# Kernel optimization log

Measured on AMD Instinct MI355X. Metric: run time of the kernel, lower is better.

The kernel has to match this reference:

```python
import jax, jax.numpy as jnp
import numpy as np
import math

N, E, D, H, L, DIN, NEP = 20000, 320000, 128, 8, 4, 16, 4
DFF = 4 * D
DH = D // H
SCALE = 1.0 / math.sqrt(DH)


def _ln(x, s, b, eps=1e-5):
    mu = x.mean(-1, keepdims=True)
    var = ((x - mu) ** 2).mean(-1, keepdims=True)
    return (x - mu) * jax.lax.rsqrt(var + eps) * s + b


def _attn(h, src, dst, ew, Wq, Wk, Wv, Wo, Wo_b):
    n = h.shape[0]
    Q = (h @ Wq).reshape(n, H, DH)
    K = (h @ Wk).reshape(n, H, DH)
    V = (h @ Wv).reshape(n, H, DH)
    # per-edge scores: [E, H]; ew is sigmoid(edge_feat.sum(-1, keepdims)) -> [E, 1]
    scores = (Q[src] * K[dst]).sum(-1) * SCALE * ew
    msg = V[dst] * scores[:, :, None]                       # [E, H, DH]
    sums = jax.ops.segment_sum(msg, dst, num_segments=n)    # [N, H, DH]
    cnt = jax.ops.segment_sum(jnp.ones((msg.shape[0],), h.dtype), dst, num_segments=n)
    out = sums / jnp.maximum(cnt, 1.0)[:, None, None]       # segment-mean (zeros if no edges)
    return out.reshape(n, D) @ Wo + Wo_b


def setup_inputs() -> dict:
    key = jax.random.key(0)
    ks = iter(jax.random.split(key, 40))
    rn = lambda *s: jax.random.normal(next(ks), s, jnp.float32) * 0.02
    inp = {
        'x': jax.random.normal(next(ks), (N, DIN), jnp.float32),
        'edge_index': jax.random.randint(next(ks), (2, E), 0, N),
        'edge_attr': jax.random.normal(next(ks), (E, 1), jnp.float32),
        'in_w': rn(DIN, D), 'in_b': jnp.zeros((D,)),
        'ee_w1': rn(1, D // 4), 'ee_b1': jnp.zeros((D // 4,)),
        'ee_w2': rn(D // 4, D // 2), 'ee_b2': jnp.zeros((D // 2,)),
        'Wq': rn(L, D, D), 'Wk': rn(L, D, D), 'Wv': rn(L, D, D),
        'Wo': rn(L, D, D), 'Wo_b': jnp.zeros((L, D)),
        'ff_w1': rn(L, D, DFF), 'ff_b1': jnp.zeros((L, DFF)),
        'ff_w2': rn(L, DFF, D), 'ff_b2': jnp.zeros((L, D)),
        'ln1_s': jnp.ones((L, D)), 'ln1_b': jnp.zeros((L, D)),
        'ln2_s': jnp.ones((L, D)), 'ln2_b': jnp.zeros((L, D)),
        'ec_w1': rn(D * 2 + D // 2, D), 'ec_b1': jnp.zeros((D,)),
        'ec_w2': rn(D, D // 2), 'ec_b2': jnp.zeros((D // 2,)),
        'ec_w3': rn(D // 2, 1), 'ec_b3': jnp.zeros((1,)),
        'pp_w1': rn(D * 2 + D // 2, D), 'pp_b1': jnp.zeros((D,)),
        'pp_w2': rn(D, D // 2), 'pp_b2': jnp.zeros((D // 2,)),
        'pp_w3': rn(D // 2, NEP), 'pp_b3': jnp.zeros((NEP,)),
    }
    return inp


def reference(x, edge_index, edge_attr, in_w, in_b, ee_w1, ee_b1, ee_w2, ee_b2,
              Wq, Wk, Wv, Wo, Wo_b, ff_w1, ff_b1, ff_w2, ff_b2,
              ln1_s, ln1_b, ln2_s, ln2_b,
              ec_w1, ec_b1, ec_w2, ec_b2, ec_w3, ec_b3,
              pp_w1, pp_b1, pp_w2, pp_b2, pp_w3, pp_b3):
    src, dst = edge_index[0], edge_index[1]
    h = x @ in_w + in_b                                     # [N, D]
    edge_feat = jax.nn.relu(edge_attr @ ee_w1 + ee_b1) @ ee_w2 + ee_b2  # [E, D/2]
    ew = jax.nn.sigmoid(edge_feat.sum(-1, keepdims=True))   # [E, 1]
    for l in range(L):
        a = _attn(h, src, dst, ew, Wq[l], Wk[l], Wv[l], Wo[l], Wo_b[l])
        h = _ln(h + a, ln1_s[l], ln1_b[l])
        f = jax.nn.relu(h @ ff_w1[l] + ff_b1[l]) @ ff_w2[l] + ff_b2[l]
        h = _ln(h + f, ln2_s[l], ln2_b[l])
    ef = jnp.concatenate([h[src], h[dst], edge_feat], axis=1)  # [E, 2.5*D]
    z = jax.nn.relu(ef @ ec_w1 + ec_b1)
    z = jax.nn.relu(z @ ec_w2 + ec_b2)
    edge_logits = (z @ ec_w3 + ec_b3).squeeze(-1)
    p = jax.nn.relu(ef @ pp_w1 + pp_b1)
    p = jax.nn.relu(p @ pp_w2 + pp_b2)
    edge_params = jax.nn.softplus(p @ pp_w3 + pp_b3) + 1e-6
    return edge_logits, edge_params
```

## Files before the change

### kernel.cpp

```cpp
#include <hip/hip_runtime.h>
#include <hip/hip_bf16.h>
#include <math.h>

#define N_NODES 20000
#define N_EDGES 320000
#define D 128
#define DFF 512
#define DIN 16
#define NLAYER 4
#define SCALE 0.25f
#define KE1 288

typedef __hip_bfloat16 bf16;
typedef __attribute__((ext_vector_type(8))) __bf16 bf16x8_t;
typedef __attribute__((ext_vector_type(4))) float f32x4;

__global__ void k_input_proj(const float* __restrict__ x, const float* __restrict__ in_w,
                             const float* __restrict__ in_b, float* __restrict__ h,
                             __bf16* __restrict__ h_bf) {
  int node = blockIdx.x;
  int j = threadIdx.x;
  __shared__ float xs[DIN];
  if (j < DIN) xs[j] = x[node * DIN + j];
  __syncthreads();
  float acc = in_b[j];
  for (int k = 0; k < DIN; ++k) acc = fmaf(xs[k], in_w[k * D + j], acc);
  h[(size_t)node * D + j] = acc;
  h_bf[(size_t)node * D + j] = (__bf16)acc;
}

__global__ void k_edge_prep(const float* __restrict__ ea, const float* __restrict__ w1,
                            const float* __restrict__ b1, const float* __restrict__ w2,
                            const float* __restrict__ b2, const int* __restrict__ dst,
                            float* __restrict__ ew, float* __restrict__ cnt) {
  __shared__ float rs[32], w1s[32], b1s[32];
  __shared__ float b2sum;
  int tid = threadIdx.x;
  if (tid < 32) {
    float s = 0.f;
    for (int j = 0; j < 64; ++j) s += w2[tid * 64 + j];
    rs[tid] = s;
    w1s[tid] = w1[tid];
    b1s[tid] = b1[tid];
  }
  if (tid == 0) {
    float s = 0.f;
    for (int j = 0; j < 64; ++j) s += b2[j];
    b2sum = s;
  }
  __syncthreads();
  int e = blockIdx.x * blockDim.x + tid;
  if (e >= N_EDGES) return;
  float a = ea[e];
  float s = b2sum;
  for (int i = 0; i < 32; ++i) {
    float t = fmaxf(fmaf(a, w1s[i], b1s[i]), 0.f);
    s = fmaf(t, rs[i], s);
  }
  ew[e] = 1.f / (1.f + expf(-s));
  atomicAdd(&cnt[dst[e]], 1.f);
}

__global__ void k_cvt_all(const float* __restrict__ Wq, const float* __restrict__ Wk,
                          const float* __restrict__ Wv, const float* __restrict__ ffw1,
                          const float* __restrict__ ffw2, const float* __restrict__ Wo,
                          const float* __restrict__ ecw2, const float* __restrict__ ppw2,
                          __bf16* __restrict__ wqkvT, __bf16* __restrict__ w1T,
                          __bf16* __restrict__ w2T, __bf16* __restrict__ woT,
                          __bf16* __restrict__ w2ET, __bf16* __restrict__ w2PT) {
  int t = blockIdx.x * 256 + threadIdx.x;
  if (t < 196608) {
    int l = t / 49152, u = t % 49152;
    int m = u / 16384, v = u % 16384;
    int n = v / 128, k = v % 128;
    const float* W = (m == 0) ? Wq : (m == 1) ? Wk : Wv;
    wqkvT[t] = (__bf16)W[l * 16384 + k * 128 + n];
  } else if (t < 196608 + 262144) {
    int u = t - 196608;
    int l = u / 65536, v = u % 65536;
    int n = v / 128, k = v % 128;
    w1T[u] = (__bf16)ffw1[l * 65536 + k * 512 + n];
  } else if (t < 458752 + 262144) {
    int u = t - 458752;
    int l = u / 65536, v = u % 65536;
    int n = v / 512, k = v % 512;
    w2T[u] = (__bf16)ffw2[l * 65536 + k * 128 + n];
  } else if (t < 720896 + 65536) {
    int u = t - 720896;
    int l = u / 16384, v = u % 16384;
    int n = v / 128, k = v % 128;
    woT[u] = (__bf16)Wo[l * 16384 + k * 128 + n];
  } else if (t < 786432 + 8192) {
    int u = t - 786432;
    int n = u / 128, k = u % 128;
    w2ET[u] = (__bf16)ecw2[k * 64 + n];
  } else if (t < 794624 + 8192) {
    int u = t - 794624;
    int n = u / 128, k = u % 128;
    w2PT[u] = (__bf16)ppw2[k * 64 + n];
  }
}

__global__ void k_prep(const float* __restrict__ ec_w1, const float* __restrict__ ec_b1,
                       const float* __restrict__ pp_w1, const float* __restrict__ pp_b1,
                       const float* __restrict__ ee_w2, const float* __restrict__ ee_b2,
                       __bf16* __restrict__ w1ET, __bf16* __restrict__ w1PT,
                       float* __restrict__ b1Ep, float* __restrict__ b1Pp) {
  int tid = threadIdx.x;
  int p = tid >> 7, n = tid & 127;
  const float* w1 = p ? pp_w1 : ec_w1;
  const float* bb = p ? pp_b1 : ec_b1;
  __bf16* wT = p ? w1PT : w1ET;
  float* bo = p ? b1Pp : b1Ep;
  for (int k = 0; k < 256; ++k) wT[n * KE1 + k] = (__bf16)w1[k * 128 + n];
  for (int i = 0; i < 32; ++i) {
    float m = 0.f;
    for (int j = 0; j < 64; ++j) m = fmaf(ee_w2[i * 64 + j], w1[(256 + j) * 128 + n], m);
    wT[n * KE1 + 256 + i] = (__bf16)m;
  }
  float b = bb[n];
  for (int j = 0; j < 64; ++j) b = fmaf(ee_b2[j], w1[(256 + j) * 128 + n], b);
  bo[n] = b;
}

__global__ __launch_bounds__(256) void k_qkv(const __bf16* __restrict__ h_bf,
                                             const __bf16* __restrict__ wT,
                                             __bf16* __restrict__ Q, __bf16* __restrict__ K,
                                             __bf16* __restrict__ V) {
  int tid = threadIdx.x, wv = tid >> 6, lane = tid & 63;
  int lr = lane & 15, lk = (lane >> 4) * 8, g4 = (lane >> 4) * 4;
  int n0 = blockIdx.x * 16;
  const __bf16* hp = h_bf + (size_t)(n0 + lr) * D;
  f32x4 acc[6];
#pragma unroll
  for (int j = 0; j < 6; ++j) acc[j] = (f32x4){0.f, 0.f, 0.f, 0.f};
#pragma unroll
  for (int ks = 0; ks < 4; ++ks) {
    bf16x8_t aF = *(const bf16x8_t*)&hp[ks * 32 + lk];
#pragma unroll
    for (int j = 0; j < 6; ++j) {
      int nb = wv * 6 + j;
      bf16x8_t bF = *(const bf16x8_t*)&wT[(nb * 16 + lr) * 128 + ks * 32 + lk];
      acc[j] = __builtin_amdgcn_mfma_f32_16x16x32_bf16(aF, bF, acc[j], 0, 0, 0);
    }
  }
#pragma unroll
  for (int j = 0; j < 6; ++j) {
    int nb = wv * 6 + j;
    int m = nb >> 3;
    __bf16* out = (m == 0) ? Q : (m == 1) ? K : V;
#pragma unroll
    for (int r = 0; r < 4; ++r)
      out[(size_t)(n0 + g4 + r) * D + (nb & 7) * 16 + lr] = (__bf16)acc[j][r];
  }
}

__global__ void k_edge_attn(const int* __restrict__ src, const int* __restrict__ dst,
                            const float* __restrict__ ew, const __bf16* __restrict__ Q,
                            const __bf16* __restrict__ K, float* __restrict__ sc) {
  int t = blockIdx.x * blockDim.x + threadIdx.x;
  if (t >= N_EDGES * 8) return;
  int e = t >> 3, hd = t & 7;
  int s = src[e], d = dst[e];
  const __bf16* q = Q + (size_t)s * D + hd * 16;
  const __bf16* k = K + (size_t)d * D + hd * 16;
  bf16x8_t q0 = *(const bf16x8_t*)q, q1 = *(const bf16x8_t*)(q + 8);
  bf16x8_t k0 = *(const bf16x8_t*)k, k1 = *(const bf16x8_t*)(k + 8);
  float p = 0.f;
#pragma unroll
  for (int i = 0; i < 8; ++i) p = fmaf((float)q0[i], (float)k0[i], p);
#pragma unroll
  for (int i = 0; i < 8; ++i) p = fmaf((float)q1[i], (float)k1[i], p);
  atomicAdd(&sc[d * 8 + hd], p * SCALE * ew[e]);
}

__global__ __launch_bounds__(256) void k_node(
    float* __restrict__ sc, const float* __restrict__ cnt, const __bf16* __restrict__ Vin,
    float* __restrict__ h, __bf16* __restrict__ h_bf, const __bf16* __restrict__ woT,
    const float* __restrict__ Wo_b, const float* __restrict__ ln1_s,
    const float* __restrict__ ln1_b, const __bf16* __restrict__ w1T,
    const __bf16* __restrict__ w2T, const float* __restrict__ b1,
    const float* __restrict__ b2, const float* __restrict__ ln2_s,
    const float* __restrict__ ln2_b, const __bf16* __restrict__ wqkvT_next,
    __bf16* __restrict__ Q, __bf16* __restrict__ K, __bf16* __restrict__ Vout) {
  __shared__ __bf16 z0[16][136];
  __shared__ __bf16 z1[16][520];
  __shared__ float lnb[4][16][2];
  int tid = threadIdx.x, wv = tid >> 6, lane = tid & 63;
  int lr = lane & 15, lk = (lane >> 4) * 8, g4 = (lane >> 4) * 4;
  int n0 = blockIdx.x * 16;
  int nd = n0 + lr;

  float inv = 1.f / fmaxf(cnt[nd], 1.f);
  float scs[8];
#pragma unroll
  for (int i = 0; i < 8; ++i) scs[i] = sc[nd * 8 + i] * inv;
  f32x4 acc[2];
#pragma unroll
  for (int j = 0; j < 2; ++j) {
    float bv = Wo_b[(wv * 2 + j) * 16 + lr];
    acc[j] = (f32x4){bv, bv, bv, bv};
  }
#pragma unroll
  for (int ks = 0; ks < 4; ++ks) {
    bf16x8_t v8 = *(const bf16x8_t*)&Vin[(size_t)nd * D + ks * 32 + lk];
    float m = scs[(ks * 32 + lk) >> 4];
    bf16x8_t aF;
#pragma unroll
    for (int i = 0; i < 8; ++i) aF[i] = (__bf16)((float)v8[i] * m);
#pragma unroll
    for (int j = 0; j < 2; ++j) {
      bf16x8_t bF = *(const bf16x8_t*)&woT[((wv * 2 + j) * 16 + lr) * 128 + ks * 32 + lk];
      acc[j] = __builtin_amdgcn_mfma_f32_16x16x32_bf16(aF, bF, acc[j], 0, 0, 0);
    }
  }
  float y[2][4];
#pragma unroll
  for (int j = 0; j < 2; ++j)
#pragma unroll
    for (int r = 0; r < 4; ++r)
      y[j][r] = h[(size_t)(n0 + g4 + r) * D + (wv * 2 + j) * 16 + lr] + acc[j][r];
  float s_[4], q_[4];
#pragma unroll
  for (int r = 0; r < 4; ++r) {
    float a0 = y[0][r], a1 = y[1][r];
    float s = a0 + a1, q = fmaf(a0, a0, a1 * a1);
    s += __shfl_xor(s, 1); s += __shfl_xor(s, 2); s += __shfl_xor(s, 4); s += __shfl_xor(s, 8);
    q += __shfl_xor(q, 1); q += __shfl_xor(q, 2); q += __shfl_xor(q, 4); q += __shfl_xor(q, 8);
    s_[r] = s; q_[r] = q;
  }
  if (lr == 0) {
#pragma unroll
    for (int r = 0; r < 4; ++r) {
      lnb[wv][g4 + r][0] = s_[r];
      lnb[wv][g4 + r][1] = q_[r];
    }
  }
  __syncthreads();
  if (tid < 128) sc[n0 * 8 + tid] = 0.f;
  float mean[4], rstd[4];
#pragma unroll
  for (int r = 0; r < 4; ++r) {
    float sm = 0.f, sq = 0.f;
#pragma unroll
    for (int w2i = 0; w2i < 4; ++w2i) {
      sm += lnb[w2i][g4 + r][0];
      sq += lnb[w2i][g4 + r][1];
    }
    float mu = sm * (1.f / 128.f);
    mean[r] = mu;
    rstd[r] = rsqrtf(sq * (1.f / 128.f) - mu * mu + 1e-5f);
  }
#pragma unroll
  for (int j = 0; j < 2; ++j) {
    int col = (wv * 2 + j) * 16 + lr;
    float lsv = ln1_s[col], lbv = ln1_b[col];
#pragma unroll
    for (int r = 0; r < 4; ++r) {
      y[j][r] = (y[j][r] - mean[r]) * rstd[r] * lsv + lbv;
      z0[g4 + r][col] = (__bf16)y[j][r];
    }
  }
  __syncthreads();

  f32x4 a1[8];
#pragma unroll
  for (int j = 0; j < 8; ++j) {
    float bv = b1[(wv * 8 + j) * 16 + lr];
    a1[j] = (f32x4){bv, bv, bv, bv};
  }
#pragma unroll
  for (int ks = 0; ks < 4; ++ks) {
    bf16x8_t aF = *(const bf16x8_t*)&z0[lr][ks * 32 + lk];
#pragma unroll
    for (int j = 0; j < 8; ++j) {
      bf16x8_t bF = *(const bf16x8_t*)&w1T[((wv * 8 + j) * 16 + lr) * 128 + ks * 32 + lk];
      a1[j] = __builtin_amdgcn_mfma_f32_16x16x32_bf16(aF, bF, a1[j], 0, 0, 0);
    }
  }
#pragma unroll
  for (int j = 0; j < 8; ++j)
#pragma unroll
    for (int r = 0; r < 4; ++r)
      z1[g4 + r][(wv * 8 + j) * 16 + lr] = (__bf16)fmaxf(a1[j][r], 0.f);
  __syncthreads();

  f32x4 a2[2];
#pragma unroll
  for (int j = 0; j < 2; ++j) {
    float bv = b2[(wv * 2 + j) * 16 + lr];
    a2[j] = (f32x4){bv, bv, bv, bv};
  }
#pragma unroll
  for (int ks = 0; ks < 16; ++ks) {
    bf16x8_t aF = *(const bf16x8_t*)&z1[lr][ks * 32 + lk];
#pragma unroll
    for (int j = 0; j < 2; ++j) {
      bf16x8_t bF = *(const bf16x8_t*)&w2T[((wv * 2 + j) * 16 + lr) * 512 + ks * 32 + lk];
      a2[j] = __builtin_amdgcn_mfma_f32_16x16x32_bf16(aF, bF, a2[j], 0, 0, 0);
    }
  }
#pragma unroll
  for (int j = 0; j < 2; ++j)
#pragma unroll
    for (int r = 0; r < 4; ++r) y[j][r] += a2[j][r];
#pragma unroll
  for (int r = 0; r < 4; ++r) {
    float a0 = y[0][r], a1v = y[1][r];
    float s = a0 + a1v, q = fmaf(a0, a0, a1v * a1v);
    s += __shfl_xor(s, 1); s += __shfl_xor(s, 2); s += __shfl_xor(s, 4); s += __shfl_xor(s, 8);
    q += __shfl_xor(q, 1); q += __shfl_xor(q, 2); q += __shfl_xor(q, 4); q += __shfl_xor(q, 8);
    s_[r] = s; q_[r] = q;
  }
  if (lr == 0) {
#pragma unroll
    for (int r = 0; r < 4; ++r) {
      lnb[wv][g4 + r][0] = s_[r];
      lnb[wv][g4 + r][1] = q_[r];
    }
  }
  __syncthreads();
#pragma unroll
  for (int r = 0; r < 4; ++r) {
    float sm = 0.f, sq = 0.f;
#pragma unroll
    for (int w2i = 0; w2i < 4; ++w2i) {
      sm += lnb[w2i][g4 + r][0];
      sq += lnb[w2i][g4 + r][1];
    }
    float mu = sm * (1.f / 128.f);
    mean[r] = mu;
    rstd[r] = rsqrtf(sq * (1.f / 128.f) - mu * mu + 1e-5f);
  }
#pragma unroll
  for (int j = 0; j < 2; ++j) {
    int col = (wv * 2 + j) * 16 + lr;
    float lsv = ln2_s[col], lbv = ln2_b[col];
#pragma unroll
    for (int r = 0; r < 4; ++r) {
      float yv = (y[j][r] - mean[r]) * rstd[r] * lsv + lbv;
      y[j][r] = yv;
      h[(size_t)(n0 + g4 + r) * D + col] = yv;
      h_bf[(size_t)(n0 + g4 + r) * D + col] = (__bf16)yv;
    }
  }

  if (wqkvT_next) {
#pragma unroll
    for (int j = 0; j < 2; ++j)
#pragma unroll
      for (int r = 0; r < 4; ++r)
        z0[g4 + r][(wv * 2 + j) * 16 + lr] = (__bf16)y[j][r];
    __syncthreads();
    f32x4 aq[6];
#pragma unroll
    for (int j = 0; j < 6; ++j) aq[j] = (f32x4){0.f, 0.f, 0.f, 0.f};
#pragma unroll
    for (int ks = 0; ks < 4; ++ks) {
      bf16x8_t aF = *(const bf16x8_t*)&z0[lr][ks * 32 + lk];
#pragma unroll
      for (int j = 0; j < 6; ++j) {
        int nb = wv * 6 + j;
        bf16x8_t bF = *(const bf16x8_t*)&wqkvT_next[(nb * 16 + lr) * 128 + ks * 32 + lk];
        aq[j] = __builtin_amdgcn_mfma_f32_16x16x32_bf16(aF, bF, aq[j], 0, 0, 0);
      }
    }
#pragma unroll
    for (int j = 0; j < 6; ++j) {
      int nb = wv * 6 + j;
      int m = nb >> 3;
      __bf16* out = (m == 0) ? Q : (m == 1) ? K : Vout;
#pragma unroll
      for (int r = 0; r < 4; ++r)
        out[(size_t)(n0 + g4 + r) * D + (nb & 7) * 16 + lr] = (__bf16)aq[j][r];
    }
  }
}

__global__ __launch_bounds__(256) void k_final(
    const int* __restrict__ src, const int* __restrict__ dst, const __bf16* __restrict__ h_bf,
    const float* __restrict__ ea, const float* __restrict__ ee_w1,
    const float* __restrict__ ee_b1, const __bf16* __restrict__ w1ET,
    const __bf16* __restrict__ w1PT, const __bf16* __restrict__ w2ET,
    const __bf16* __restrict__ w2PT, const float* __restrict__ b1Ep,
    const float* __restrict__ b1Pp, const float* __restrict__ ec_b2,
    const float* __restrict__ ec_w3, const float* __restrict__ ec_b3,
    const float* __restrict__ pp_b2, const float* __restrict__ pp_w3,
    const float* __restrict__ pp_b3, float* __restrict__ out_logits,
    float* __restrict__ out_params) {
  __shared__ __bf16 z1[2][32][136];
  int tid = threadIdx.x, wv = tid >> 6, lane = tid & 63;
  int lr = lane & 15, lk = (lane >> 4) * 8, g4 = (lane >> 4) * 4;
  int p = wv & 1, m0 = (wv >> 1) * 16;
  int e0 = blockIdx.x * 32;
  int e = e0 + m0 + lr;
  int s_row = src[e], d_row = dst[e];
  float av = ea[e];
  const __bf16* hs = h_bf + (size_t)s_row * D;
  const __bf16* hd = h_bf + (size_t)d_row * D;
  bf16x8_t aR;
#pragma unroll
  for (int i = 0; i < 8; ++i)
    aR[i] = (__bf16)fmaxf(fmaf(av, ee_w1[lk + i], ee_b1[lk + i]), 0.f);

  const __bf16* w1x = p ? w1PT : w1ET;
  const float* b1x = p ? b1Pp : b1Ep;
  const __bf16* w2x = p ? w2PT : w2ET;
  const float* b2x = p ? pp_b2 : ec_b2;

  f32x4 acc[8];
#pragma unroll
  for (int nb = 0; nb < 8; ++nb) {
    float bv = b1x[nb * 16 + lr];
    acc[nb] = (f32x4){bv, bv, bv, bv};
  }
#pragma unroll
  for (int ks = 0; ks < 9; ++ks) {
    bf16x8_t aF;
    if (ks < 4)
      aF = *(const bf16x8_t*)&hs[ks * 32 + lk];
    else if (ks < 8)
      aF = *(const bf16x8_t*)&hd[(ks - 4) * 32 + lk];
    else
      aF = aR;
#pragma unroll
    for (int nb = 0; nb < 8; ++nb) {
      bf16x8_t bF = *(const bf16x8_t*)&w1x[(nb * 16 + lr) * KE1 + ks * 32 + lk];
      acc[nb] = __builtin_amdgcn_mfma_f32_16x16x32_bf16(aF, bF, acc[nb], 0, 0, 0);
    }
  }
#pragma unroll
  for (int nb = 0; nb < 8; ++nb)
#pragma unroll
    for (int r = 0; r < 4; ++r)
      z1[p][m0 + g4 + r][nb * 16 + lr] = (__bf16)fmaxf(acc[nb][r], 0.f);

  f32x4 acc2[4];
#pragma unroll
  for (int nb = 0; nb < 4; ++nb) {
    float bv = b2x[nb * 16 + lr];
    acc2[nb] = (f32x4){bv, bv, bv, bv};
  }
#pragma unroll
  for (int ks = 0; ks < 4; ++ks) {
    bf16x8_t aF = *(const bf16x8_t*)&z1[p][m0 + lr][ks * 32 + lk];
#pragma unroll
    for (int nb = 0; nb < 4; ++nb) {
      bf16x8_t bF = *(const bf16x8_t*)&w2x[(nb * 16 + lr) * 128 + ks * 32 + lk];
      acc2[nb] = __builtin_amdgcn_mfma_f32_16x16x32_bf16(aF, bF, acc2[nb], 0, 0, 0);
    }
  }

  if (p == 0) {
    float w3v[4];
#pragma unroll
    for (int nb = 0; nb < 4; ++nb) w3v[nb] = ec_w3[nb * 16 + lr];
    float b3 = ec_b3[0];
#pragma unroll
    for (int r = 0; r < 4; ++r) {
      float s = 0.f;
#pragma unroll
      for (int nb = 0; nb < 4; ++nb) s = fmaf(fmaxf(acc2[nb][r], 0.f), w3v[nb], s);
      s += __shfl_xor(s, 1);
      s += __shfl_xor(s, 2);
      s += __shfl_xor(s, 4);
      s += __shfl_xor(s, 8);
      if (lr == 0) out_logits[e0 + m0 + g4 + r] = s + b3;
    }
  } else {
    float wp[4][4];
#pragma unroll
    for (int nb = 0; nb < 4; ++nb)
#pragma unroll
      for (int c = 0; c < 4; ++c) wp[nb][c] = pp_w3[(nb * 16 + lr) * 4 + c];
#pragma unroll
    for (int c = 0; c < 4; ++c) {
      float b3 = pp_b3[c];
#pragma unroll
      for (int r = 0; r < 4; ++r) {
        float s = 0.f;
#pragma unroll
        for (int nb = 0; nb < 4; ++nb) s = fmaf(fmaxf(acc2[nb][r], 0.f), wp[nb][c], s);
        s += __shfl_xor(s, 1);
        s += __shfl_xor(s, 2);
        s += __shfl_xor(s, 4);
        s += __shfl_xor(s, 8);
        if (lr == 0) {
          float xx = s + b3;
          float sp = fmaxf(xx, 0.f) + log1pf(expf(-fabsf(xx)));
          out_params[(size_t)(e0 + m0 + g4 + r) * 4 + c] = sp + 1e-6f;
        }
      }
    }
  }
}

extern "C" void kernel_launch(void* const* d_in, const int* in_sizes, int n_in,
                              void* d_out, int out_size, void* d_ws, size_t ws_size,
                              hipStream_t stream) {
  const float* x = (const float*)d_in[0];
  const int* eidx = (const int*)d_in[1];
  const float* eattr = (const float*)d_in[2];
  const float* in_w = (const float*)d_in[3];
  const float* in_b = (const float*)d_in[4];
  const float* ee_w1 = (const float*)d_in[5];
  const float* ee_b1 = (const float*)d_in[6];
  const float* ee_w2 = (const float*)d_in[7];
  const float* ee_b2 = (const float*)d_in[8];
  const float* Wq = (const float*)d_in[9];
  const float* Wk = (const float*)d_in[10];
  const float* Wv = (const float*)d_in[11];
  const float* Wo = (const float*)d_in[12];
  const float* Wo_b = (const float*)d_in[13];
  const float* ff_w1 = (const float*)d_in[14];
  const float* ff_b1 = (const float*)d_in[15];
  const float* ff_w2 = (const float*)d_in[16];
  const float* ff_b2 = (const float*)d_in[17];
  const float* ln1_s = (const float*)d_in[18];
  const float* ln1_b = (const float*)d_in[19];
  const float* ln2_s = (const float*)d_in[20];
  const float* ln2_b = (const float*)d_in[21];
  const float* ec_w1 = (const float*)d_in[22];
  const float* ec_b1 = (const float*)d_in[23];
  const float* ec_w2 = (const float*)d_in[24];
  const float* ec_b2 = (const float*)d_in[25];
  const float* ec_w3 = (const float*)d_in[26];
  const float* ec_b3 = (const float*)d_in[27];
  const float* pp_w1 = (const float*)d_in[28];
  const float* pp_b1 = (const float*)d_in[29];
  const float* pp_w2 = (const float*)d_in[30];
  const float* pp_b2 = (const float*)d_in[31];
  const float* pp_w3 = (const float*)d_in[32];
  const float* pp_b3 = (const float*)d_in[33];

  const int* src = eidx;
  const int* dst = eidx + N_EDGES;

  char* wsb = (char*)d_ws;
  float* sc = (float*)wsb;
  float* cnt = (float*)(wsb + 640000);
  float* h = (float*)(wsb + 720000);
  __bf16* h_bf = (__bf16*)(wsb + 10960000);
  __bf16* Q = (__bf16*)(wsb + 16080000);
  __bf16* Kb = (__bf16*)(wsb + 21200000);
  __bf16* V0 = (__bf16*)(wsb + 26320000);
  __bf16* V1 = (__bf16*)(wsb + 31440000);
  float* ew = (float*)(wsb + 36560000);
  __bf16* wqkvT = (__bf16*)(wsb + 37840000);
  __bf16* w1T = (__bf16*)(wsb + 38233216);
  __bf16* w2T = (__bf16*)(wsb + 38757504);
  __bf16* woT = (__bf16*)(wsb + 39281792);
  __bf16* w1ET = (__bf16*)(wsb + 39412864);
  __bf16* w1PT = (__bf16*)(wsb + 39486592);
  __bf16* w2ET = (__bf16*)(wsb + 39560320);
  __bf16* w2PT = (__bf16*)(wsb + 39576704);
  float* b1Ep = (float*)(wsb + 39593088);
  float* b1Pp = (float*)(wsb + 39593600);

  hipMemsetAsync(cnt, 0, N_NODES * sizeof(float), stream);
  hipMemsetAsync(sc, 0, N_NODES * 8 * sizeof(float), stream);
  k_input_proj<<<N_NODES, D, 0, stream>>>(x, in_w, in_b, h, h_bf);
  k_edge_prep<<<(N_EDGES + 255) / 256, 256, 0, stream>>>(eattr, ee_w1, ee_b1, ee_w2, ee_b2,
                                                         dst, ew, cnt);
  k_cvt_all<<<(802816 + 255) / 256, 256, 0, stream>>>(Wq, Wk, Wv, ff_w1, ff_w2, Wo, ec_w2,
                                                      pp_w2, wqkvT, w1T, w2T, woT, w2ET, w2PT);
  k_prep<<<1, 256, 0, stream>>>(ec_w1, ec_b1, pp_w1, pp_b1, ee_w2, ee_b2, w1ET, w1PT, b1Ep,
                                b1Pp);

  int nblk = N_NODES / 16;
  k_qkv<<<nblk, 256, 0, stream>>>(h_bf, wqkvT, Q, Kb, V0);
  for (int l = 0; l < NLAYER; ++l) {
    __bf16* Vin = (l & 1) ? V1 : V0;
    __bf16* Vout = (l & 1) ? V0 : V1;
    k_edge_attn<<<(N_EDGES * 8 + 255) / 256, 256, 0, stream>>>(src, dst, ew, Q, Kb, sc);
    k_node<<<nblk, 256, 0, stream>>>(
        sc, cnt, Vin, h, h_bf, woT + (size_t)l * 16384, Wo_b + l * D, ln1_s + l * D,
        ln1_b + l * D, w1T + (size_t)l * 65536, w2T + (size_t)l * 65536, ff_b1 + l * DFF,
        ff_b2 + l * D, ln2_s + l * D, ln2_b + l * D,
        (l < NLAYER - 1) ? (wqkvT + (size_t)(l + 1) * 49152) : (const __bf16*)nullptr, Q, Kb,
        Vout);
  }

  float* out_logits = (float*)d_out;
  float* out_params = out_logits + N_EDGES;
  k_final<<<N_EDGES / 32, 256, 0, stream>>>(src, dst, h_bf, eattr, ee_w1, ee_b1, w1ET, w1PT,
                                            w2ET, w2PT, b1Ep, b1Pp, ec_b2, ec_w3, ec_b3,
                                            pp_b2, pp_w3, pp_b3, out_logits, out_params);
}
```

Before: 743.1 us.

## Precompute per-node first-layer projections for edge MLP heads before gathering

The first layer of the edge-classifier and parameter heads is split by linearity: h[src]@W_src and h[dst]@W_dst are computed once per node in a new k_pnode kernel, and k_final gathers and sums these projected rows instead of running a 288-wide GEMM per edge. This cuts the first-layer MFMA work per edge from nine K-steps to one (the edge-feature part only), at the cost of an extra node-level kernel and the gather traffic. The precomputed projections reuse the Q/K/V buffers as scratch, and rounding the partial sums to bf16 before adding them slightly changes numerics.

```diff
diff --git a/kernel.cpp b/kernel.cpp
--- a/kernel.cpp
+++ b/kernel.cpp
@@ -377,27 +377,59 @@
   }
 }
 
+__global__ __launch_bounds__(256) void k_pnode(const __bf16* __restrict__ h_bf,
+                                               const __bf16* __restrict__ w1ET,
+                                               const __bf16* __restrict__ w1PT,
+                                               __bf16* __restrict__ PsE,
+                                               __bf16* __restrict__ PdE,
+                                               __bf16* __restrict__ PsP,
+                                               __bf16* __restrict__ PdP) {
+  int tid = threadIdx.x, wv = tid >> 6, lane = tid & 63;
+  int lr = lane & 15, lk = (lane >> 4) * 8, g4 = (lane >> 4) * 4;
+  int n0 = blockIdx.x * 16;
+  const __bf16* hp = h_bf + (size_t)(n0 + lr) * D;
+  const __bf16* wsrc = (wv & 2) ? w1PT : w1ET;
+  int koff = (wv & 1) ? 128 : 0;
+  __bf16* out = (wv == 0) ? PsE : (wv == 1) ? PdE : (wv == 2) ? PsP : PdP;
+  f32x4 acc[8];
+#pragma unroll
+  for (int nb = 0; nb < 8; ++nb) acc[nb] = (f32x4){0.f, 0.f, 0.f, 0.f};
+#pragma unroll
+  for (int ks = 0; ks < 4; ++ks) {
+    bf16x8_t aF = *(const bf16x8_t*)&hp[ks * 32 + lk];
+#pragma unroll
+    for (int nb = 0; nb < 8; ++nb) {
+      bf16x8_t bF = *(const bf16x8_t*)&wsrc[(nb * 16 + lr) * KE1 + koff + ks * 32 + lk];
+      acc[nb] = __builtin_amdgcn_mfma_f32_16x16x32_bf16(aF, bF, acc[nb], 0, 0, 0);
+    }
+  }
+#pragma unroll
+  for (int nb = 0; nb < 8; ++nb)
+#pragma unroll
+    for (int r = 0; r < 4; ++r)
+      out[(size_t)(n0 + g4 + r) * D + nb * 16 + lr] = (__bf16)acc[nb][r];
+}
+
 __global__ __launch_bounds__(256) void k_final(
-    const int* __restrict__ src, const int* __restrict__ dst, const __bf16* __restrict__ h_bf,
-    const float* __restrict__ ea, const float* __restrict__ ee_w1,
-    const float* __restrict__ ee_b1, const __bf16* __restrict__ w1ET,
-    const __bf16* __restrict__ w1PT, const __bf16* __restrict__ w2ET,
-    const __bf16* __restrict__ w2PT, const float* __restrict__ b1Ep,
-    const float* __restrict__ b1Pp, const float* __restrict__ ec_b2,
-    const float* __restrict__ ec_w3, const float* __restrict__ ec_b3,
-    const float* __restrict__ pp_b2, const float* __restrict__ pp_w3,
-    const float* __restrict__ pp_b3, float* __restrict__ out_logits,
-    float* __restrict__ out_params) {
+    const int* __restrict__ src, const int* __restrict__ dst, const float* __restrict__ ea,
+    const float* __restrict__ ee_w1, const float* __restrict__ ee_b1,
+    const __bf16* __restrict__ w1ET, const __bf16* __restrict__ w1PT,
+    const __bf16* __restrict__ w2ET, const __bf16* __restrict__ w2PT,
+    const float* __restrict__ b1Ep, const float* __restrict__ b1Pp,
+    const __bf16* __restrict__ PsE, const __bf16* __restrict__ PdE,
+    const __bf16* __restrict__ PsP, const __bf16* __restrict__ PdP,
+    const float* __restrict__ ec_b2, const float* __restrict__ ec_w3,
+    const float* __restrict__ ec_b3, const float* __restrict__ pp_b2,
+    const float* __restrict__ pp_w3, const float* __restrict__ pp_b3,
+    float* __restrict__ out_logits, float* __restrict__ out_params) {
   __shared__ __bf16 z1[2][32][136];
+  __shared__ __bf16 zf[4][16][136];
   int tid = threadIdx.x, wv = tid >> 6, lane = tid & 63;
   int lr = lane & 15, lk = (lane >> 4) * 8, g4 = (lane >> 4) * 4;
   int p = wv & 1, m0 = (wv >> 1) * 16;
   int e0 = blockIdx.x * 32;
   int e = e0 + m0 + lr;
-  int s_row = src[e], d_row = dst[e];
   float av = ea[e];
-  const __bf16* hs = h_bf + (size_t)s_row * D;
-  const __bf16* hd = h_bf + (size_t)d_row * D;
   bf16x8_t aR;
 #pragma unroll
   for (int i = 0; i < 8; ++i)
@@ -415,25 +447,34 @@
     acc[nb] = (f32x4){bv, bv, bv, bv};
   }
 #pragma unroll
-  for (int ks = 0; ks < 9; ++ks) {
-    bf16x8_t aF;
-    if (ks < 4)
-      aF = *(const bf16x8_t*)&hs[ks * 32 + lk];
-    else if (ks < 8)
-      aF = *(const bf16x8_t*)&hd[(ks - 4) * 32 + lk];
-    else
-      aF = aR;
-#pragma unroll
-    for (int nb = 0; nb < 8; ++nb) {
-      bf16x8_t bF = *(const bf16x8_t*)&w1x[(nb * 16 + lr) * KE1 + ks * 32 + lk];
-      acc[nb] = __builtin_amdgcn_mfma_f32_16x16x32_bf16(aF, bF, acc[nb], 0, 0, 0);
-    }
+  for (int nb = 0; nb < 8; ++nb) {
+    bf16x8_t bF = *(const bf16x8_t*)&w1x[(nb * 16 + lr) * KE1 + 256 + lk];
+    acc[nb] = __builtin_amdgcn_mfma_f32_16x16x32_bf16(aR, bF, acc[nb], 0, 0, 0);
   }
 #pragma unroll
   for (int nb = 0; nb < 8; ++nb)
 #pragma unroll
-    for (int r = 0; r < 4; ++r)
-      z1[p][m0 + g4 + r][nb * 16 + lr] = (__bf16)fmaxf(acc[nb][r], 0.f);
+    for (int r = 0; r < 4; ++r) zf[wv][g4 + r][nb * 16 + lr] = (__bf16)acc[nb][r];
+
+  {
+    int em = lane >> 2, c4 = lane & 3;
+    int ee = e0 + m0 + em;
+    const __bf16* Ps = p ? PsP : PsE;
+    const __bf16* Pd = p ? PdP : PdE;
+    const __bf16* psrow = Ps + (size_t)src[ee] * D + c4 * 32;
+    const __bf16* pdrow = Pd + (size_t)dst[ee] * D + c4 * 32;
+#pragma unroll
+    for (int ch = 0; ch < 4; ++ch) {
+      bf16x8_t a = *(const bf16x8_t*)&psrow[ch * 8];
+      bf16x8_t b = *(const bf16x8_t*)&pdrow[ch * 8];
+      bf16x8_t f = *(const bf16x8_t*)&zf[wv][em][c4 * 32 + ch * 8];
+      bf16x8_t o;
+#pragma unroll
+      for (int i = 0; i < 8; ++i)
+        o[i] = (__bf16)fmaxf((float)a[i] + (float)b[i] + (float)f[i], 0.f);
+      *(bf16x8_t*)&z1[p][m0 + em][c4 * 32 + ch * 8] = o;
+    }
+  }
 
   f32x4 acc2[4];
 #pragma unroll
@@ -581,9 +622,16 @@
         Vout);
   }
 
+  __bf16* PsE = Q;
+  __bf16* PdE = Kb;
+  __bf16* PsP = V0;
+  __bf16* PdP = V1;
+  k_pnode<<<nblk, 256, 0, stream>>>(h_bf, w1ET, w1PT, PsE, PdE, PsP, PdP);
+
   float* out_logits = (float*)d_out;
   float* out_params = out_logits + N_EDGES;
-  k_final<<<N_EDGES / 32, 256, 0, stream>>>(src, dst, h_bf, eattr, ee_w1, ee_b1, w1ET, w1PT,
-                                            w2ET, w2PT, b1Ep, b1Pp, ec_b2, ec_w3, ec_b3,
-                                            pp_b2, pp_w3, pp_b3, out_logits, out_params);
-}
+  k_final<<<N_EDGES / 32, 256, 0, stream>>>(src, dst, eattr, ee_w1, ee_b1, w1ET, w1PT, w2ET,
+                                            w2PT, b1Ep, b1Pp, PsE, PdE, PsP, PdP, ec_b2,
+                                            ec_w3, ec_b3, pp_b2, pp_w3, pp_b3, out_logits,
+                                            out_params);
+}
```

Result: faster. 615.3 us (-17.2%).
